# Kernel tuning notes

Hardware: AMD Instinct MI355X
Metric: run time of the kernel (lower is better)

## Reference

```python
import jax, jax.numpy as jnp
import numpy as np

N = 100000   # nodes
E = 1000000  # edges (avg degree 10)
F_IN, H1, H2, C = 128, 64, 64, 16


def setup_inputs() -> dict:
    key = jax.random.key(0)
    ks = jax.random.split(key, 10)
    x = jax.random.normal(ks[0], (N, F_IN), dtype=jnp.float32)
    edge_src = jax.random.randint(ks[1], (E,), 0, N, dtype=jnp.int32)
    edge_dst = jax.random.randint(ks[2], (E,), 0, N, dtype=jnp.int32)
    # normalized-adjacency-like positive edge weights (~1/deg scale)
    edge_val = jax.random.uniform(ks[3], (E,), dtype=jnp.float32) * 0.1
    def glorot(k, fan_in, fan_out):
        s = np.float32(1.0 / np.sqrt(fan_in))
        return jax.random.normal(k, (fan_in, fan_out), dtype=jnp.float32) * s
    W1 = glorot(ks[4], F_IN, H1)
    W2 = glorot(ks[5], H1, H2)
    W3 = glorot(ks[6], H2, C)
    b1 = jnp.zeros((H1,), jnp.float32)
    b2 = jnp.zeros((H2,), jnp.float32)
    b3 = jnp.zeros((C,), jnp.float32)
    return {"x": x, "edge_val": edge_val, "W1": W1, "b1": b1,
            "W2": W2, "b2": b2, "W3": W3, "b3": b3,
            "edge_src": edge_src, "edge_dst": edge_dst}


def gcn_layer(h, W, b, edge_src, edge_dst, edge_val):
    # support = h @ W ; out = spmm(adj, support) + b
    support = h @ W                                  # [N, d_out]
    msg = support[edge_src] * edge_val[:, None]      # [E, d_out] gather + scale
    agg = jax.ops.segment_sum(msg, edge_dst, num_segments=N)  # scatter-add
    return agg + b


def reference(x, edge_val, W1, b1, W2, b2, W3, b3, edge_src, edge_dst):
    # eval mode: F.dropout(training=False) is identity
    h = jax.nn.relu(gcn_layer(x, W1, b1, edge_src, edge_dst, edge_val))
    h = jax.nn.relu(gcn_layer(h, W2, b2, edge_src, edge_dst, edge_val))
    return gcn_layer(h, W3, b3, edge_src, edge_dst, edge_val)  # [N, C] logits
```

## Files before the change

kernel.cpp:

```cpp
#include <hip/hip_runtime.h>
#include <stdint.h>

#define N_NODES 100000
#define N_EDGES 1000000
#define NBUCK 98

typedef __attribute__((ext_vector_type(8))) __bf16 bf16x8;
typedef __attribute__((ext_vector_type(4))) float f32x4;

static __device__ __forceinline__ float bf2f(unsigned short u) {
    return __uint_as_float(((unsigned int)u) << 16);
}
static __device__ __forceinline__ unsigned short f2bf(float f) {
    unsigned int u = __float_as_uint(f);
    unsigned int r = (u + 0x7FFFu + ((u >> 16) & 1u)) >> 16;
    return (unsigned short)r;
}
static __device__ __forceinline__ float4 ld4_half(const unsigned short* p) {
    ushort4 u = *(const ushort4*)p;
    return make_float4(bf2f(u.x), bf2f(u.y), bf2f(u.z), bf2f(u.w));
}
static __device__ __forceinline__ void st4_half(unsigned short* p, float4 f) {
    ushort4 u;
    u.x = f2bf(f.x); u.y = f2bf(f.y); u.z = f2bf(f.z); u.w = f2bf(f.w);
    *(ushort4*)p = u;
}

static __device__ __forceinline__ float ldf(const void* p, size_t i, int bf) {
    return bf ? bf2f(((const unsigned short*)p)[i]) : ((const float*)p)[i];
}
static __device__ __forceinline__ float4 ldf4(const void* p, size_t i, int bf) {
    if (bf) return ld4_half((const unsigned short*)p + i);
    return *(const float4*)((const float*)p + i);
}

__global__ __launch_bounds__(256) void detect_kernel(const unsigned short* __restrict__ xs,
                                                     int* __restrict__ flag) {
    __shared__ int sz;
    if (threadIdx.x == 0) sz = 0;
    __syncthreads();
    int z = 0;
    for (int i = threadIdx.x; i < 1024; i += 256) {
        float av = fabsf(bf2f(xs[2 * i]));
        if (!(av <= 1048576.0f) || (av != 0.0f && av < 9.5367431640625e-07f)) z++;
    }
    atomicAdd(&sz, z);
    __syncthreads();
    if (threadIdx.x == 0) *flag = (sz > 256) ? 0 : 1;
}

__global__ __launch_bounds__(256) void bhist_kernel(const int* __restrict__ dst,
                                                    int* __restrict__ bcount) {
    __shared__ int cnt[NBUCK];
    int tid = threadIdx.x;
    for (int i = tid; i < NBUCK; i += 256) cnt[i] = 0;
    __syncthreads();
    int e0 = blockIdx.x * 4096;
#pragma unroll
    for (int i = 0; i < 16; ++i) {
        int e = e0 + i * 256 + tid;
        if (e < N_EDGES) atomicAdd(&cnt[dst[e] >> 10], 1);
    }
    __syncthreads();
    for (int i = tid; i < NBUCK; i += 256) {
        int c = cnt[i];
        if (c) atomicAdd(&bcount[i], c);
    }
}

__global__ __launch_bounds__(128) void bscan_kernel(const int* __restrict__ bcount,
                                                    int* __restrict__ bstart,
                                                    int* __restrict__ bcursor) {
    __shared__ int sh[128];
    int tid = threadIdx.x;
    int v = (tid < NBUCK) ? bcount[tid] : 0;
    sh[tid] = v;
    __syncthreads();
    for (int off = 1; off < 128; off <<= 1) {
        int t = 0;
        if (tid >= off) t = sh[tid - off];
        __syncthreads();
        if (tid >= off) sh[tid] += t;
        __syncthreads();
    }
    if (tid < NBUCK) {
        int excl = sh[tid] - v;
        bstart[tid] = excl;
        bcursor[tid] = excl;
    }
    if (tid == NBUCK - 1) bstart[NBUCK] = sh[tid];
}

__global__ __launch_bounds__(256) void part_kernel(const int* __restrict__ src,
                                                   const int* __restrict__ dst,
                                                   const void* __restrict__ val,
                                                   int* __restrict__ bcursor,
                                                   int2* __restrict__ part,
                                                   const int* __restrict__ flagp) {
    __shared__ int cnt[NBUCK];
    __shared__ int base[NBUCK];
    const int bf = *flagp;
    const int tid = threadIdx.x;
    const int e0 = blockIdx.x * 2048;
    for (int i = tid; i < NBUCK; i += 256) cnt[i] = 0;
    __syncthreads();
    int rank[8], bkt[8], pk[8], vb[8];
#pragma unroll
    for (int i = 0; i < 8; ++i) {
        int e = e0 + i * 256 + tid;
        bkt[i] = -1;
        if (e < N_EDGES) {
            int d = dst[e];
            int b = d >> 10;
            bkt[i] = b;
            pk[i] = src[e] | ((d & 1023) << 17);
            vb[i] = __float_as_int(ldf(val, e, bf));
            rank[i] = atomicAdd(&cnt[b], 1);
        }
    }
    __syncthreads();
    for (int i = tid; i < NBUCK; i += 256) {
        int c = cnt[i];
        base[i] = c ? atomicAdd(&bcursor[i], c) : 0;
    }
    __syncthreads();
#pragma unroll
    for (int i = 0; i < 8; ++i) {
        if (bkt[i] >= 0) part[(size_t)base[bkt[i]] + rank[i]] = make_int2(pk[i], vb[i]);
    }
}

__global__ __launch_bounds__(512) void place_kernel(const int* __restrict__ bstart,
                                                    const int2* __restrict__ part,
                                                    int* __restrict__ row_start,
                                                    int2* __restrict__ csr_rec) {
    __shared__ int cnt[1024];
    __shared__ int sums[512];
    const int tid = threadIdx.x;
    const int b = blockIdx.x;
    const int row0 = b << 10;
    const int nrows = min(1024, N_NODES - row0);
    const int s = bstart[b], e = bstart[b + 1];

    for (int i = tid; i < 1024; i += 512) cnt[i] = 0;
    __syncthreads();
    for (int j = s + tid; j < e; j += 512) {
        unsigned p = (unsigned)part[j].x;
        atomicAdd(&cnt[p >> 17], 1);
    }
    __syncthreads();
    int a0 = cnt[2 * tid], a1 = cnt[2 * tid + 1];
    int ts = a0 + a1;
    sums[tid] = ts;
    __syncthreads();
    for (int off = 1; off < 512; off <<= 1) {
        int t = 0;
        if (tid >= off) t = sums[tid - off];
        __syncthreads();
        if (tid >= off) sums[tid] += t;
        __syncthreads();
    }
    int excl = sums[tid] - ts;
    cnt[2 * tid] = s + excl;
    cnt[2 * tid + 1] = s + excl + a0;
    if (2 * tid < nrows)     row_start[row0 + 2 * tid] = s + excl;
    if (2 * tid + 1 < nrows) row_start[row0 + 2 * tid + 1] = s + excl + a0;
    if (b == NBUCK - 1 && tid == 0) row_start[N_NODES] = e;
    __syncthreads();
    for (int j = s + tid; j < e; j += 512) {
        int2 r = part[j];
        unsigned p = (unsigned)r.x;
        int pos = atomicAdd(&cnt[p >> 17], 1);
        csr_rec[pos] = make_int2((int)(p & 0x1FFFFu), r.y);
    }
}

static __device__ __forceinline__ void row_gather_u(const unsigned short* __restrict__ supc,
                                                    const int2* __restrict__ csr_rec,
                                                    int s, int e, int M,
                                                    float& a0, float& a1, float& a2, float& a3) {
    if (s >= e) return;
    int2 r[8];
#pragma unroll
    for (int t = 0; t < 8; ++t) r[t] = csr_rec[min(s + t, e - 1)];
    for (int j = s; j < e; j += 8) {
        float4 sp[8];
#pragma unroll
        for (int t = 0; t < 8; ++t) sp[t] = ld4_half(supc + (size_t)r[t].x * M);
        float v[8];
#pragma unroll
        for (int t = 0; t < 8; ++t) v[t] = (j + t < e) ? __int_as_float(r[t].y) : 0.0f;
        int jn = j + 8;
        if (jn < e) {
#pragma unroll
            for (int t = 0; t < 8; ++t) r[t] = csr_rec[min(jn + t, e - 1)];
        }
#pragma unroll
        for (int t = 0; t < 8; ++t) {
            a0 += v[t] * sp[t].x; a1 += v[t] * sp[t].y;
            a2 += v[t] * sp[t].z; a3 += v[t] * sp[t].w;
        }
    }
}

template <int K, int M, bool DYNIN>
__global__ __launch_bounds__(256, 4) void mgemm_kernel(const void* __restrict__ hv_,
                                                       const void* __restrict__ W,
                                                       unsigned short* __restrict__ out,
                                                       const int* __restrict__ flagp) {
    constexpr int KP = K + 8;
    constexpr int NC = M / 16;
    constexpr int NK = K / 32;
    constexpr int NT = (N_NODES + 63) / 64;

    __shared__ unsigned short wt[M][KP];

    const int bf = *flagp;
    const int tid = threadIdx.x;

    for (int i = tid; i < K * M; i += 256) {
        int k = i / M, m = i % M;
        wt[m][k] = f2bf(ldf(W, i, bf));
    }
    __syncthreads();

    const int lane = tid & 63;
    const int qd = lane >> 4;
    const int ln = lane & 15;
    const int wrow = (tid >> 6) * 16;

    for (int tile = blockIdx.x; tile < NT; tile += gridDim.x) {
        const int row = tile * 64 + wrow + ln;
        const bool ok = row < N_NODES;

        f32x4 acc[NC];
#pragma unroll
        for (int c = 0; c < NC; ++c) acc[c] = (f32x4){0.f, 0.f, 0.f, 0.f};

#pragma unroll
        for (int ks = 0; ks < NK; ++ks) {
            bf16x8 a;
            if (ok) {
                const size_t base = (size_t)row * K + ks * 32 + qd * 8;
                if (DYNIN && !bf) {
                    const float* xp = (const float*)hv_ + base;
                    float4 f0 = *(const float4*)xp;
                    float4 f1 = *(const float4*)(xp + 4);
                    ushort4 uu[2];
                    uu[0].x = f2bf(f0.x); uu[0].y = f2bf(f0.y); uu[0].z = f2bf(f0.z); uu[0].w = f2bf(f0.w);
                    uu[1].x = f2bf(f1.x); uu[1].y = f2bf(f1.y); uu[1].z = f2bf(f1.z); uu[1].w = f2bf(f1.w);
                    a = *(const bf16x8*)uu;
                } else {
                    a = *(const bf16x8*)((const unsigned short*)hv_ + base);
                }
            } else {
                a = (bf16x8)(__bf16)0.0f;
            }
#pragma unroll
            for (int c = 0; c < NC; ++c) {
                bf16x8 b = *(const bf16x8*)&wt[c * 16 + ln][ks * 32 + qd * 8];
                acc[c] = __builtin_amdgcn_mfma_f32_16x16x32_bf16(a, b, acc[c], 0, 0, 0);
            }
        }

#pragma unroll
        for (int c = 0; c < NC; ++c) {
#pragma unroll
            for (int r = 0; r < 4; ++r) {
                int orow = tile * 64 + wrow + qd * 4 + r;
                if (orow < N_NODES) out[(size_t)orow * M + c * 16 + ln] = f2bf(acc[c][r]);
            }
        }
    }
}

template <int MOUT>
__global__ __launch_bounds__(256, 4) void fused_kernel(const unsigned short* __restrict__ support,
                                                       const int* __restrict__ row_start,
                                                       const int2* __restrict__ csr_rec,
                                                       const void* __restrict__ bias,
                                                       const void* __restrict__ W,
                                                       unsigned short* __restrict__ out,
                                                       const int* __restrict__ flagp) {
    constexpr int K = 64, KP = 72;
    constexpr int NC = MOUT / 16;
    constexpr int NK = 2;
    constexpr int NT = (N_NODES + 63) / 64;

    __shared__ unsigned short agg[64][KP];
    __shared__ unsigned short wt[MOUT][KP];

    const int bf = *flagp;
    const int tid = threadIdx.x;

    for (int i = tid; i < K * MOUT; i += 256) {
        int k = i / MOUT, m = i % MOUT;
        wt[m][k] = f2bf(ldf(W, i, bf));
    }
    __syncthreads();

    const int lane = tid & 63;
    const int qd = lane >> 4;
    const int ln = lane & 15;
    const int wrow = (tid >> 6) * 16;

    const int grp = tid >> 4;
    const int cc = tid & 15;
    const float bs0 = ldf(bias, cc * 4 + 0, bf);
    const float bs1 = ldf(bias, cc * 4 + 1, bf);
    const float bs2 = ldf(bias, cc * 4 + 2, bf);
    const float bs3 = ldf(bias, cc * 4 + 3, bf);
    const unsigned short* supc = support + cc * 4;

    for (int tile = blockIdx.x; tile < NT; tile += gridDim.x) {
#pragma unroll
        for (int rr = 0; rr < 4; ++rr) {
            int rl = grp * 4 + rr;
            int row = tile * 64 + rl;
            float a0 = bs0, a1 = bs1, a2 = bs2, a3 = bs3;
            if (row < N_NODES) {
                int s = row_start[row];
                int e = row_start[row + 1];
                row_gather_u(supc, csr_rec, s, e, 64, a0, a1, a2, a3);
                a0 = fmaxf(a0, 0.f); a1 = fmaxf(a1, 0.f);
                a2 = fmaxf(a2, 0.f); a3 = fmaxf(a3, 0.f);
            } else {
                a0 = a1 = a2 = a3 = 0.f;
            }
            st4_half(&agg[rl][cc * 4], make_float4(a0, a1, a2, a3));
        }
        __syncthreads();

        f32x4 acc[NC];
#pragma unroll
        for (int c = 0; c < NC; ++c) acc[c] = (f32x4){0.f, 0.f, 0.f, 0.f};
#pragma unroll
        for (int ks = 0; ks < NK; ++ks) {
            bf16x8 a = *(const bf16x8*)&agg[wrow + ln][ks * 32 + qd * 8];
#pragma unroll
            for (int c = 0; c < NC; ++c) {
                bf16x8 b = *(const bf16x8*)&wt[c * 16 + ln][ks * 32 + qd * 8];
                acc[c] = __builtin_amdgcn_mfma_f32_16x16x32_bf16(a, b, acc[c], 0, 0, 0);
            }
        }

#pragma unroll
        for (int c = 0; c < NC; ++c) {
#pragma unroll
            for (int r = 0; r < 4; ++r) {
                int orow = tile * 64 + wrow + qd * 4 + r;
                if (orow < N_NODES) out[(size_t)orow * MOUT + c * 16 + ln] = f2bf(acc[c][r]);
            }
        }
        __syncthreads();
    }
}

template <bool DYNOUT>
__global__ __launch_bounds__(256) void spmm16_kernel(const unsigned short* __restrict__ support,
                                                     const int* __restrict__ row_start,
                                                     const int2* __restrict__ csr_rec,
                                                     const void* __restrict__ bias,
                                                     void* __restrict__ out_,
                                                     const int* __restrict__ flagp) {
    constexpr int M = 16;
    int bf = *flagp;
    int tid = threadIdx.x;
    int gid = blockIdx.x * 64 + tid / 4;
    int c0 = (tid % 4) * 4;
    if (gid >= N_NODES) return;
    int s = row_start[gid];
    int e = row_start[gid + 1];
    float a0 = ldf(bias, c0 + 0, bf);
    float a1 = ldf(bias, c0 + 1, bf);
    float a2 = ldf(bias, c0 + 2, bf);
    float a3 = ldf(bias, c0 + 3, bf);
    row_gather_u(support + c0, csr_rec, s, e, M, a0, a1, a2, a3);
    float4 f = make_float4(a0, a1, a2, a3);
    if (DYNOUT && !bf) *(float4*)((float*)out_ + (size_t)gid * M + c0) = f;
    else               st4_half((unsigned short*)out_ + (size_t)gid * M + c0, f);
}

extern "C" void kernel_launch(void* const* d_in, const int* in_sizes, int n_in,
                              void* d_out, int out_size, void* d_ws, size_t ws_size,
                              hipStream_t stream) {
    (void)in_sizes; (void)n_in; (void)out_size; (void)ws_size;
    const void* x  = d_in[0];
    const void* ev = d_in[1];
    const void* W1 = d_in[2];
    const void* b1 = d_in[3];
    const void* W2 = d_in[4];
    const void* b2 = d_in[5];
    const void* W3 = d_in[6];
    const void* b3 = d_in[7];
    const int* esrc = (const int*)d_in[8];
    const int* edst = (const int*)d_in[9];

    char* ws = (char*)d_ws;
    size_t off = 0;
    auto alloc = [&](size_t bytes) -> void* {
        void* p = ws + off;
        off = (off + bytes + 255) & ~(size_t)255;
        return p;
    };
    unsigned short* A = (unsigned short*)alloc((size_t)N_NODES * 64 * 2);
    unsigned short* B = (unsigned short*)alloc((size_t)N_NODES * 64 * 2);
    int* row_start  = (int*)alloc((size_t)(N_NODES + 1) * 4);
    int* bcount     = (int*)alloc(512);
    int* bstart     = (int*)alloc(512);
    int* bcursor    = (int*)alloc(512);
    int2* csr_rec   = (int2*)alloc((size_t)N_EDGES * 8);
    int* flagp      = (int*)alloc(256);
    int2* part      = (int2*)A;

    detect_kernel<<<1, 256, 0, stream>>>((const unsigned short*)x, flagp);

    hipMemsetAsync(bcount, 0, 512, stream);
    bhist_kernel<<<(N_EDGES + 4095) / 4096, 256, 0, stream>>>(edst, bcount);
    bscan_kernel<<<1, 128, 0, stream>>>(bcount, bstart, bcursor);
    part_kernel<<<(N_EDGES + 2047) / 2048, 256, 0, stream>>>(esrc, edst, ev, bcursor, part, flagp);
    place_kernel<<<NBUCK, 512, 0, stream>>>(bstart, part, row_start, csr_rec);

    mgemm_kernel<128, 64, true><<<1024, 256, 0, stream>>>(x, W1, A, flagp);
    fused_kernel<64><<<1024, 256, 0, stream>>>(A, row_start, csr_rec, b1, W2, B, flagp);
    fused_kernel<16><<<1024, 256, 0, stream>>>(B, row_start, csr_rec, b2, W3, A, flagp);
    spmm16_kernel<true><<<(N_NODES + 63) / 64, 256, 0, stream>>>(A, row_start, csr_rec, b3, d_out, flagp);
}
```

Baseline: 262.0 us.

## Gather four consecutive CSR rows per thread group as one merged edge stream

```diff
diff --git a/kernel.cpp b/kernel.cpp
--- a/kernel.cpp
+++ b/kernel.cpp
@@ -175,10 +175,11 @@
     }
 }
 
-static __device__ __forceinline__ void row_gather_u(const unsigned short* __restrict__ supc,
-                                                    const int2* __restrict__ csr_rec,
-                                                    int s, int e, int M,
-                                                    float& a0, float& a1, float& a2, float& a3) {
+template <int M>
+static __device__ __forceinline__ void quad_gather(const unsigned short* __restrict__ supc,
+                                                   const int2* __restrict__ csr_rec,
+                                                   int s, int b1, int b2, int b3, int e,
+                                                   float4 acc[4]) {
     if (s >= e) return;
     int2 r[8];
 #pragma unroll
@@ -187,9 +188,9 @@
         float4 sp[8];
 #pragma unroll
         for (int t = 0; t < 8; ++t) sp[t] = ld4_half(supc + (size_t)r[t].x * M);
-        float v[8];
-#pragma unroll
-        for (int t = 0; t < 8; ++t) v[t] = (j + t < e) ? __int_as_float(r[t].y) : 0.0f;
+        float wv[8];
+#pragma unroll
+        for (int t = 0; t < 8; ++t) wv[t] = (j + t < e) ? __int_as_float(r[t].y) : 0.0f;
         int jn = j + 8;
         if (jn < e) {
 #pragma unroll
@@ -197,8 +198,18 @@
         }
 #pragma unroll
         for (int t = 0; t < 8; ++t) {
-            a0 += v[t] * sp[t].x; a1 += v[t] * sp[t].y;
-            a2 += v[t] * sp[t].z; a3 += v[t] * sp[t].w;
+            int idx = j + t;
+            float c0 = (idx < b1) ? wv[t] : 0.0f;
+            float c1 = (idx < b2) ? wv[t] : 0.0f;
+            float c2 = (idx < b3) ? wv[t] : 0.0f;
+            float w0 = c0;
+            float w1 = c1 - c0;
+            float w2 = c2 - c1;
+            float w3 = wv[t] - c2;
+            acc[0].x += w0 * sp[t].x; acc[0].y += w0 * sp[t].y; acc[0].z += w0 * sp[t].z; acc[0].w += w0 * sp[t].w;
+            acc[1].x += w1 * sp[t].x; acc[1].y += w1 * sp[t].y; acc[1].z += w1 * sp[t].z; acc[1].w += w1 * sp[t].w;
+            acc[2].x += w2 * sp[t].x; acc[2].y += w2 * sp[t].y; acc[2].z += w2 * sp[t].z; acc[2].w += w2 * sp[t].w;
+            acc[3].x += w3 * sp[t].x; acc[3].y += w3 * sp[t].y; acc[3].z += w3 * sp[t].z; acc[3].w += w3 * sp[t].w;
         }
     }
 }
@@ -275,13 +286,13 @@
 }
 
 template <int MOUT>
-__global__ __launch_bounds__(256, 4) void fused_kernel(const unsigned short* __restrict__ support,
-                                                       const int* __restrict__ row_start,
-                                                       const int2* __restrict__ csr_rec,
-                                                       const void* __restrict__ bias,
-                                                       const void* __restrict__ W,
-                                                       unsigned short* __restrict__ out,
-                                                       const int* __restrict__ flagp) {
+__global__ __launch_bounds__(256) void fused_kernel(const unsigned short* __restrict__ support,
+                                                    const int* __restrict__ row_start,
+                                                    const int2* __restrict__ csr_rec,
+                                                    const void* __restrict__ bias,
+                                                    const void* __restrict__ W,
+                                                    unsigned short* __restrict__ out,
+                                                    const int* __restrict__ flagp) {
     constexpr int K = 64, KP = 72;
     constexpr int NC = MOUT / 16;
     constexpr int NK = 2;
@@ -306,41 +317,39 @@
 
     const int grp = tid >> 4;
     const int cc = tid & 15;
-    const float bs0 = ldf(bias, cc * 4 + 0, bf);
-    const float bs1 = ldf(bias, cc * 4 + 1, bf);
-    const float bs2 = ldf(bias, cc * 4 + 2, bf);
-    const float bs3 = ldf(bias, cc * 4 + 3, bf);
+    const float4 bias4 = make_float4(ldf(bias, cc * 4 + 0, bf), ldf(bias, cc * 4 + 1, bf),
+                                     ldf(bias, cc * 4 + 2, bf), ldf(bias, cc * 4 + 3, bf));
     const unsigned short* supc = support + cc * 4;
 
     for (int tile = blockIdx.x; tile < NT; tile += gridDim.x) {
-#pragma unroll
-        for (int rr = 0; rr < 4; ++rr) {
-            int rl = grp * 4 + rr;
-            int row = tile * 64 + rl;
-            float a0 = bs0, a1 = bs1, a2 = bs2, a3 = bs3;
-            if (row < N_NODES) {
-                int s = row_start[row];
-                int e = row_start[row + 1];
-                row_gather_u(supc, csr_rec, s, e, 64, a0, a1, a2, a3);
-                a0 = fmaxf(a0, 0.f); a1 = fmaxf(a1, 0.f);
-                a2 = fmaxf(a2, 0.f); a3 = fmaxf(a3, 0.f);
-            } else {
-                a0 = a1 = a2 = a3 = 0.f;
-            }
-            st4_half(&agg[rl][cc * 4], make_float4(a0, a1, a2, a3));
-        }
-        __syncthreads();
-
-        f32x4 acc[NC];
-#pragma unroll
-        for (int c = 0; c < NC; ++c) acc[c] = (f32x4){0.f, 0.f, 0.f, 0.f};
+        const int r0 = tile * 64 + grp * 4;
+        int s  = row_start[min(r0 + 0, N_NODES)];
+        int b1 = row_start[min(r0 + 1, N_NODES)];
+        int b2 = row_start[min(r0 + 2, N_NODES)];
+        int b3 = row_start[min(r0 + 3, N_NODES)];
+        int e  = row_start[min(r0 + 4, N_NODES)];
+
+        float4 acc[4] = {bias4, bias4, bias4, bias4};
+        quad_gather<64>(supc, csr_rec, s, b1, b2, b3, e, acc);
+#pragma unroll
+        for (int k = 0; k < 4; ++k) {
+            float4 a = acc[k];
+            a.x = fmaxf(a.x, 0.f); a.y = fmaxf(a.y, 0.f);
+            a.z = fmaxf(a.z, 0.f); a.w = fmaxf(a.w, 0.f);
+            st4_half(&agg[grp * 4 + k][cc * 4], a);
+        }
+        __syncthreads();
+
+        f32x4 macc[NC];
+#pragma unroll
+        for (int c = 0; c < NC; ++c) macc[c] = (f32x4){0.f, 0.f, 0.f, 0.f};
 #pragma unroll
         for (int ks = 0; ks < NK; ++ks) {
             bf16x8 a = *(const bf16x8*)&agg[wrow + ln][ks * 32 + qd * 8];
 #pragma unroll
             for (int c = 0; c < NC; ++c) {
                 bf16x8 b = *(const bf16x8*)&wt[c * 16 + ln][ks * 32 + qd * 8];
-                acc[c] = __builtin_amdgcn_mfma_f32_16x16x32_bf16(a, b, acc[c], 0, 0, 0);
+                macc[c] = __builtin_amdgcn_mfma_f32_16x16x32_bf16(a, b, macc[c], 0, 0, 0);
             }
         }
 
@@ -349,7 +358,7 @@
 #pragma unroll
             for (int r = 0; r < 4; ++r) {
                 int orow = tile * 64 + wrow + qd * 4 + r;
-                if (orow < N_NODES) out[(size_t)orow * MOUT + c * 16 + ln] = f2bf(acc[c][r]);
+                if (orow < N_NODES) out[(size_t)orow * MOUT + c * 16 + ln] = f2bf(macc[c][r]);
             }
         }
         __syncthreads();
@@ -366,19 +375,27 @@
     constexpr int M = 16;
     int bf = *flagp;
     int tid = threadIdx.x;
-    int gid = blockIdx.x * 64 + tid / 4;
-    int c0 = (tid % 4) * 4;
-    if (gid >= N_NODES) return;
-    int s = row_start[gid];
-    int e = row_start[gid + 1];
-    float a0 = ldf(bias, c0 + 0, bf);
-    float a1 = ldf(bias, c0 + 1, bf);
-    float a2 = ldf(bias, c0 + 2, bf);
-    float a3 = ldf(bias, c0 + 3, bf);
-    row_gather_u(support + c0, csr_rec, s, e, M, a0, a1, a2, a3);
-    float4 f = make_float4(a0, a1, a2, a3);
-    if (DYNOUT && !bf) *(float4*)((float*)out_ + (size_t)gid * M + c0) = f;
-    else               st4_half((unsigned short*)out_ + (size_t)gid * M + c0, f);
+    int grp = tid >> 2;
+    int cc = tid & 3;
+    int r0 = blockIdx.x * 256 + grp * 4;
+    if (r0 >= N_NODES) return;
+    int s  = row_start[min(r0 + 0, N_NODES)];
+    int b1 = row_start[min(r0 + 1, N_NODES)];
+    int b2 = row_start[min(r0 + 2, N_NODES)];
+    int b3 = row_start[min(r0 + 3, N_NODES)];
+    int e  = row_start[min(r0 + 4, N_NODES)];
+    float4 bias4 = make_float4(ldf(bias, cc * 4 + 0, bf), ldf(bias, cc * 4 + 1, bf),
+                               ldf(bias, cc * 4 + 2, bf), ldf(bias, cc * 4 + 3, bf));
+    float4 acc[4] = {bias4, bias4, bias4, bias4};
+    quad_gather<16>(support + cc * 4, csr_rec, s, b1, b2, b3, e, acc);
+#pragma unroll
+    for (int k = 0; k < 4; ++k) {
+        int row = r0 + k;
+        if (row < N_NODES) {
+            if (DYNOUT && !bf) *(float4*)((float*)out_ + (size_t)row * M + cc * 4) = acc[k];
+            else               st4_half((unsigned short*)out_ + (size_t)row * M + cc * 4, acc[k]);
+        }
+    }
 }
 
 extern "C" void kernel_launch(void* const* d_in, const int* in_sizes, int n_in,
@@ -424,5 +441,5 @@
     mgemm_kernel<128, 64, true><<<1024, 256, 0, stream>>>(x, W1, A, flagp);
     fused_kernel<64><<<1024, 256, 0, stream>>>(A, row_start, csr_rec, b1, W2, B, flagp);
     fused_kernel<16><<<1024, 256, 0, stream>>>(B, row_start, csr_rec, b2, W3, A, flagp);
-    spmm16_kernel<true><<<(N_NODES + 63) / 64, 256, 0, stream>>>(A, row_start, csr_rec, b3, d_out, flagp);
-}
+    spmm16_kernel<true><<<(N_NODES + 255) / 256, 256, 0, stream>>>(A, row_start, csr_rec, b3, d_out, flagp);
+}
```

After: 258.7 us. No clear change (-1.2%).
